# Performance work log

Hardware: AMD Instinct MI355X
Metric: run time of the kernel (lower is better)

Reference implementation:

```python
import jax, jax.numpy as jnp
import numpy as np

C_Q = 256
C_KV = 256
C_HID = 32
N_HEADS = 8
INF = 1e9


def setup_inputs() -> dict:
    key = jax.random.key(0)
    ks = jax.random.split(key, 9)
    B, Q, KV = 4, 2048, 2048
    d = N_HEADS * C_HID
    glorot_q = (6.0 / (C_Q + d)) ** 0.5
    glorot_kv = (6.0 / (C_KV + d)) ** 0.5
    return {
        "input_q": jax.random.normal(ks[0], (B, Q, C_Q), dtype=jnp.float32),
        "input_kv": jax.random.normal(ks[1], (B, KV, C_KV), dtype=jnp.float32),
        "mask": jax.random.randint(ks[2], (B, 1, 1, KV), 0, 2).astype(jnp.float32),
        "bias": jax.random.normal(ks[3], (1, N_HEADS, Q, KV), dtype=jnp.float32),
        "w_q": jax.random.uniform(ks[4], (C_Q, d), jnp.float32, -glorot_q, glorot_q),
        "w_k": jax.random.uniform(ks[5], (C_KV, d), jnp.float32, -glorot_kv, glorot_kv),
        "w_v": jax.random.uniform(ks[6], (C_KV, d), jnp.float32, -glorot_kv, glorot_kv),
        "w_o": jnp.zeros((d, C_Q), dtype=jnp.float32),  # 'final' init -> zeros
        "b_o": jnp.zeros((C_Q,), dtype=jnp.float32),
    }


def reference(input_q, input_kv, mask, bias, w_q, w_k, w_v, w_o, b_o):
    B, Q, _ = input_q.shape
    KV = input_kv.shape[1]
    # project and split heads: [B, H, L, c]
    q = (input_q @ w_q).reshape(B, Q, N_HEADS, C_HID).transpose(0, 2, 1, 3)
    k = (input_kv @ w_k).reshape(B, KV, N_HEADS, C_HID).transpose(0, 2, 1, 3)
    v = (input_kv @ w_v).reshape(B, KV, N_HEADS, C_HID).transpose(0, 2, 1, 3)
    q = q / jnp.sqrt(jnp.asarray(C_HID, q.dtype))
    # scores [B, H, Q, KV] with mask-bias and additive bias before softmax
    a = jnp.einsum("bhqc,bhkc->bhqk", q, k)
    a = a + (mask - 1.0) * INF
    if bias is not None:
        a = a + bias
    a = jax.nn.softmax(a, axis=-1)
    out = jnp.einsum("bhqk,bhkc->bhqc", a, v)  # [B, H, Q, c]
    out = out.transpose(0, 2, 1, 3).reshape(B, Q, N_HEADS * C_HID)
    return out @ w_o + b_o
```

## Files before the change

### kernel.cpp

```cpp
#include <hip/hip_runtime.h>
#include <hip/hip_bf16.h>
#include <math.h>

#define B    4
#define QL   2048
#define KVL  2048
#define CQ   256
#define CKV  256
#define CH   32
#define NH   8
#define DM   256
#define QB   128
#define KVB  128
#define NSPLIT 2
#define NS2  (KVL / KVB / NSPLIT)
#define BH   (B * NH)

typedef __attribute__((ext_vector_type(8)))  short short8;
typedef __attribute__((ext_vector_type(4)))  float f32x4;
typedef __attribute__((ext_vector_type(16))) float f32x16;
typedef __attribute__((ext_vector_type(4)))  unsigned int u32x4;

static __device__ __forceinline__ short f2bf(float x) {
    __hip_bfloat16 h = __float2bfloat16(x);
    return __builtin_bit_cast(short, h);
}
static __device__ __forceinline__ unsigned int pkbf(float lo, float hi) {
    return (unsigned int)(unsigned short)f2bf(lo) |
           ((unsigned int)(unsigned short)f2bf(hi) << 16);
}

__global__ __launch_bounds__(256) void prep_cvt(
    const float* __restrict__ src, short* __restrict__ dst, int n8)
{
    int i = blockIdx.x * 256 + threadIdx.x;
    if (i >= n8) return;
    const float4* s = (const float4*)src + (size_t)i * 2;
    float4 a = s[0], b = s[1];
    short8 o = { f2bf(a.x), f2bf(a.y), f2bf(a.z), f2bf(a.w),
                 f2bf(b.x), f2bf(b.y), f2bf(b.z), f2bf(b.w) };
    *((short8*)dst + i) = o;
}

__global__ __launch_bounds__(256) void prep_wT(
    const float* __restrict__ w, short* __restrict__ wt, int K, int N)
{
    __shared__ float tile[32][33];
    const int bx = blockIdx.x * 32;
    const int by = blockIdx.y * 32;
    const int tx = threadIdx.x & 31, ty = threadIdx.x >> 5;
    #pragma unroll
    for (int i = 0; i < 32; i += 8)
        tile[ty + i][tx] = w[(size_t)(by + ty + i) * N + bx + tx];
    __syncthreads();
    #pragma unroll
    for (int i = 0; i < 32; i += 8)
        wt[(size_t)(bx + ty + i) * K + by + tx] = f2bf(tile[tx][ty + i]);
}

__global__ __launch_bounds__(256) void gemm_mfma(
    const short* __restrict__ A, const short* __restrict__ BT,
    const float* __restrict__ bias, float* __restrict__ outf,
    short* __restrict__ outb,
    int M, int N, int K, float alpha, int mode)
{
    __shared__ __align__(16) short As[64][40];
    __shared__ __align__(16) short Bs[64][40];

    const int t   = threadIdx.x;
    const int m0  = blockIdx.y * 64, n0 = blockIdx.x * 64;
    const int lane = t & 63, w = t >> 6;
    const int c16 = lane & 15, g = lane >> 4;
    const int wm  = (w & 1) * 32, wn = (w >> 1) * 32;
    const int lr  = t >> 2, lc = (t & 3) * 8;

    f32x4 acc[2][2] = {};

    for (int k0 = 0; k0 < K; k0 += 32) {
        __syncthreads();
        *(short8*)&As[lr][lc] = *(const short8*)(A  + (size_t)(m0 + lr) * K + k0 + lc);
        *(short8*)&Bs[lr][lc] = *(const short8*)(BT + (size_t)(n0 + lr) * K + k0 + lc);
        __syncthreads();

        short8 af[2], bf[2];
        #pragma unroll
        for (int i = 0; i < 2; i++) {
            af[i] = *(const short8*)&As[wm + i * 16 + c16][g * 8];
            bf[i] = *(const short8*)&Bs[wn + i * 16 + c16][g * 8];
        }
        #pragma unroll
        for (int i = 0; i < 2; i++)
            #pragma unroll
            for (int j = 0; j < 2; j++)
                acc[i][j] = __builtin_amdgcn_mfma_f32_16x16x32_bf16(af[i], bf[j], acc[i][j], 0, 0, 0);
    }

    #pragma unroll
    for (int i = 0; i < 2; i++) {
        #pragma unroll
        for (int j = 0; j < 2; j++) {
            #pragma unroll
            for (int r = 0; r < 4; r++) {
                int m = m0 + wm + i * 16 + g * 4 + r;
                int n = n0 + wn + j * 16 + c16;
                float v = acc[i][j][r] * alpha;
                if (mode == 0) {
                    outf[(size_t)m * N + n] = v + (bias ? bias[n] : 0.0f);
                } else {
                    int bb = m >> 11, l = m & 2047;
                    int hh = n >> 5,  cc = n & 31;
                    if (mode == 1)
                        outb[(((size_t)bb * NH + hh) * QL + l) * CH + cc] = f2bf(v);
                    else
                        outb[(((size_t)bb * NH + hh) * CH + cc) * (size_t)KVL + l] = f2bf(v);
                }
            }
        }
    }
}

__global__ __launch_bounds__(256) void fattn(
    const short* __restrict__ qbf, const short* __restrict__ kbf,
    const short* __restrict__ vtb, const float* __restrict__ mask,
    const float* __restrict__ bias, float* __restrict__ opart,
    float* __restrict__ lpart)
{
    __shared__ __align__(16) short Kl[2][KVB * 32];
    __shared__ __align__(16) short Vl[2][32 * KVB];
    __shared__ __align__(16) float Ml[KVL / NSPLIT];

    const int t    = threadIdx.x;
    const int wv   = t >> 6;
    const int lane = t & 63;
    const int l31  = lane & 31;
    const int hi   = lane >> 5;

    const int s  = blockIdx.x & 1;
    const int q0 = (blockIdx.x >> 1) * QB;
    const int h  = blockIdx.y, b = blockIdx.z;
    const int bh = b * NH + h;
    const int kvbase = s * (KVL / NSPLIT);

    constexpr float L2E  = 1.4426950408889634f;
    constexpr float MBIG = 1e9f * L2E;
    constexpr float MOFF = -(1e9f * L2E) - 40.0f * L2E;

    const short* qrow = qbf + ((size_t)bh * QL + q0 + wv * 32 + l31) * CH;
    short8 qf0 = *(const short8*)(qrow + hi * 8);
    short8 qf1 = *(const short8*)(qrow + 16 + hi * 8);

    {
        float4 mv = *(const float4*)(mask + (size_t)b * KVL + kvbase + t * 4);
        float4 o0 = { fmaf(mv.x, MBIG, MOFF), fmaf(mv.y, MBIG, MOFF),
                      fmaf(mv.z, MBIG, MOFF), fmaf(mv.w, MBIG, MOFF) };
        *(float4*)&Ml[t * 4] = o0;
    }

    const int rowK = t >> 1, halfK = t & 1;
    const short* ksrc = kbf + (size_t)bh * KVL * CH + (size_t)(kvbase + rowK) * CH + halfK * 16;
    const int kb0 = (rowK * 64 + halfK * 32)      ^ ((rowK & 7) << 4);
    const int kb1 = (rowK * 64 + halfK * 32 + 16) ^ ((rowK & 7) << 4);
    const int rowV = t >> 3, segV = t & 7;
    const short* vsrc = vtb + (size_t)bh * CH * KVL + (size_t)rowV * KVL + kvbase + segV * 16;
    const int vb0 = (rowV * 256 + segV * 32)      ^ ((rowV & 7) << 4);
    const int vb1 = (rowV * 256 + segV * 32 + 16) ^ ((rowV & 7) << 4);

    short8 kr0 = *(const short8*)ksrc;
    short8 kr1 = *(const short8*)(ksrc + 8);
    short8 vr0 = *(const short8*)vsrc;
    short8 vr1 = *(const short8*)(vsrc + 8);

    const float* brow = bias + ((size_t)h * QL + q0 + wv * 32 + l31) * KVL + kvbase;

    float4 biA[4], biB[4];
    #pragma unroll
    for (int rr = 0; rr < 4; ++rr)
        biA[rr] = *(const float4*)(brow + rr * 8 + hi * 4);

    f32x16 O;
    #pragma unroll
    for (int r = 0; r < 16; ++r) O[r] = 0.0f;
    float lp0 = 0.f, lp1 = 0.f, lp2 = 0.f, lp3 = 0.f;

#define SUB_BODY(SUB, BC, BN)                                                  \
    {                                                                          \
        if ((SUB) < 3 || it + 1 < NS2) {                                       \
            _Pragma("unroll")                                                  \
            for (int rr = 0; rr < 4; ++rr)                                     \
                BN[rr] = *(const float4*)(brow + kv0 + ((SUB) + 1) * 32 + rr * 8 + hi * 4); \
        }                                                                      \
        f32x16 Cb;                                                             \
        _Pragma("unroll")                                                      \
        for (int rr = 0; rr < 4; ++rr) {                                       \
            float4 mt = *(const float4*)&Ml[kv0 + (SUB) * 32 + rr * 8 + hi * 4]; \
            Cb[4 * rr + 0] = fmaf(BC[rr].x, L2E, mt.x);                        \
            Cb[4 * rr + 1] = fmaf(BC[rr].y, L2E, mt.y);                        \
            Cb[4 * rr + 2] = fmaf(BC[rr].z, L2E, mt.z);                        \
            Cb[4 * rr + 3] = fmaf(BC[rr].w, L2E, mt.w);                        \
        }                                                                      \
        const int krow32 = (SUB) * 32 + l31;                                   \
        const int kswz   = (krow32 & 7) << 4;                                  \
        short8 ka0 = *(const short8*)(klb + ((krow32 * 64 + hi * 16) ^ kswz)); \
        short8 ka1 = *(const short8*)(klb + ((krow32 * 64 + 32 + hi * 16) ^ kswz)); \
        __builtin_amdgcn_s_setprio(1);                                         \
        f32x16 S = __builtin_amdgcn_mfma_f32_32x32x16_bf16(ka0, qf0, Cb, 0, 0, 0); \
        S = __builtin_amdgcn_mfma_f32_32x32x16_bf16(ka1, qf1, S, 0, 0, 0);     \
        __builtin_amdgcn_s_setprio(0);                                         \
        float p[16];                                                           \
        _Pragma("unroll")                                                      \
        for (int r = 0; r < 16; ++r) p[r] = __builtin_amdgcn_exp2f(S[r]);      \
        lp0 += (p[0] + p[1]) + (p[4] + p[5]);                                  \
        lp1 += (p[2] + p[3]) + (p[6] + p[7]);                                  \
        lp2 += (p[8] + p[9]) + (p[12] + p[13]);                                \
        lp3 += (p[10] + p[11]) + (p[14] + p[15]);                              \
        unsigned int a1 = pkbf(p[0], p[1]),   a2 = pkbf(p[2], p[3]);           \
        unsigned int b1 = pkbf(p[4], p[5]),   b2 = pkbf(p[6], p[7]);           \
        unsigned int c1 = pkbf(p[8], p[9]),   c2 = pkbf(p[10], p[11]);         \
        unsigned int d1 = pkbf(p[12], p[13]), d2 = pkbf(p[14], p[15]);         \
        asm("v_permlane32_swap_b32 %0, %1" : "+v"(a1), "+v"(b1));              \
        asm("v_permlane32_swap_b32 %0, %1" : "+v"(a2), "+v"(b2));              \
        asm("v_permlane32_swap_b32 %0, %1" : "+v"(c1), "+v"(d1));              \
        asm("v_permlane32_swap_b32 %0, %1" : "+v"(c2), "+v"(d2));              \
        u32x4 f0 = { a1, a2, b1, b2 };                                         \
        u32x4 f1 = { c1, c2, d1, d2 };                                         \
        short8 pf0 = __builtin_bit_cast(short8, f0);                           \
        short8 pf1 = __builtin_bit_cast(short8, f1);                           \
        const int vswz = (l31 & 7) << 4;                                       \
        short8 vf0 = *(const short8*)(vlb + ((l31 * 256 + (SUB) * 64 + hi * 16) ^ vswz)); \
        short8 vf1 = *(const short8*)(vlb + ((l31 * 256 + (SUB) * 64 + 32 + hi * 16) ^ vswz)); \
        __builtin_amdgcn_s_setprio(1);                                         \
        O = __builtin_amdgcn_mfma_f32_32x32x16_bf16(pf0, vf0, O, 0, 0, 0);     \
        O = __builtin_amdgcn_mfma_f32_32x32x16_bf16(pf1, vf1, O, 0, 0, 0);     \
        __builtin_amdgcn_s_setprio(0);                                         \
    }

    #pragma unroll 1
    for (int it = 0; it < NS2; ++it) {
        const int kv0 = it * KVB;
        char* klb = (char*)Kl[it & 1];
        char* vlb = (char*)Vl[it & 1];

        *(short8*)(klb + kb0) = kr0;
        *(short8*)(klb + kb1) = kr1;
        *(short8*)(vlb + vb0) = vr0;
        *(short8*)(vlb + vb1) = vr1;
        __syncthreads();

        if (it + 1 < NS2) {
            const short* kn = ksrc + (size_t)(it + 1) * KVB * CH;
            const short* vn = vsrc + (it + 1) * KVB;
            kr0 = *(const short8*)kn;  kr1 = *(const short8*)(kn + 8);
            vr0 = *(const short8*)vn;  vr1 = *(const short8*)(vn + 8);
        }

        SUB_BODY(0, biA, biB);
        SUB_BODY(1, biB, biA);
        SUB_BODY(2, biA, biB);
        SUB_BODY(3, biB, biA);
    }
#undef SUB_BODY

    float lpq = (lp0 + lp1) + (lp2 + lp3);
    lpq += __shfl_xor(lpq, 32);
    float* op = opart + (((size_t)s * BH + bh) * QL + q0 + wv * 32) * CH;
    #pragma unroll
    for (int r = 0; r < 16; ++r) {
        int q = (r & 3) + 8 * (r >> 2) + 4 * hi;
        op[(size_t)q * CH + l31] = O[r];
    }
    if (lane < 32)
        lpart[((size_t)s * BH + bh) * QL + q0 + wv * 32 + l31] = lpq;
}

__global__ __launch_bounds__(256) void combine(
    const float* __restrict__ opart, const float* __restrict__ lpart,
    short* __restrict__ aob)
{
    const size_t BHQ = (size_t)BH * QL;
    int i  = blockIdx.x * 256 + threadIdx.x;
    int c8 = i & 3;
    int q  = (i >> 2) & (QL - 1);
    int bh = i >> 13;
    int b  = bh >> 3, h = bh & 7;

    float l0 = lpart[(size_t)bh * QL + q];
    float l1 = lpart[BHQ + (size_t)bh * QL + q];
    float inv = 1.0f / (l0 + l1);

    size_t base = ((size_t)bh * QL + q) * CH + c8 * 8;
    const float4* oa = (const float4*)(opart + base);
    const float4* ob = (const float4*)(opart + BHQ * CH + base);
    float4 x0 = oa[0], x1 = oa[1];
    float4 y0 = ob[0], y1 = ob[1];
    short8 o = { f2bf((x0.x + y0.x) * inv), f2bf((x0.y + y0.y) * inv),
                 f2bf((x0.z + y0.z) * inv), f2bf((x0.w + y0.w) * inv),
                 f2bf((x1.x + y1.x) * inv), f2bf((x1.y + y1.y) * inv),
                 f2bf((x1.z + y1.z) * inv), f2bf((x1.w + y1.w) * inv) };
    *(short8*)(aob + ((size_t)b * QL + q) * DM + h * CH + c8 * 8) = o;
}

extern "C" void kernel_launch(void* const* d_in, const int* in_sizes, int n_in,
                              void* d_out, int out_size, void* d_ws, size_t ws_size,
                              hipStream_t stream)
{
    const float* input_q  = (const float*)d_in[0];
    const float* input_kv = (const float*)d_in[1];
    const float* mask     = (const float*)d_in[2];
    const float* bias     = (const float*)d_in[3];
    const float* w_q      = (const float*)d_in[4];
    const float* w_k      = (const float*)d_in[5];
    const float* w_v      = (const float*)d_in[6];
    const float* w_o      = (const float*)d_in[7];
    const float* b_o      = (const float*)d_in[8];
    float* out = (float*)d_out;

    const size_t TOK  = (size_t)B * QL;
    const size_t HEAD = (size_t)B * NH * QL * CH;

    short* qbf = (short*)d_ws;
    short* kbf = qbf + HEAD;
    short* vtb = kbf + HEAD;
    short* aob = vtb + HEAD;
    short* qx  = aob + HEAD;
    short* kvx = qx  + HEAD;
    short* wqT = kvx + HEAD;
    short* wkT = wqT + CQ * DM;
    short* wvT = wkT + CKV * DM;
    short* woT = wvT + CKV * DM;
    float* opart = (float*)(woT + DM * CQ);
    float* lpart = opart + 2 * (size_t)BH * QL * CH;

    dim3 blk(256);
    const float qscale = 0.17677669529663687f * 1.4426950408889634f;

    prep_cvt<<<dim3((TOK * CQ / 8 + 255) / 256), blk, 0, stream>>>(input_q,  qx,  (int)(TOK * CQ / 8));
    prep_cvt<<<dim3((TOK * CKV / 8 + 255) / 256), blk, 0, stream>>>(input_kv, kvx, (int)(TOK * CKV / 8));
    prep_wT<<<dim3(DM / 32, CQ / 32),  blk, 0, stream>>>(w_q, wqT, CQ,  DM);
    prep_wT<<<dim3(DM / 32, CKV / 32), blk, 0, stream>>>(w_k, wkT, CKV, DM);
    prep_wT<<<dim3(DM / 32, CKV / 32), blk, 0, stream>>>(w_v, wvT, CKV, DM);
    prep_wT<<<dim3(CQ / 32, DM / 32),  blk, 0, stream>>>(w_o, woT, DM,  CQ);

    dim3 pgrid(DM / 64, TOK / 64);
    gemm_mfma<<<pgrid, blk, 0, stream>>>(qx,  wqT, nullptr, nullptr, qbf,
                                         (int)TOK, DM, CQ,  qscale, 1);
    gemm_mfma<<<pgrid, blk, 0, stream>>>(kvx, wkT, nullptr, nullptr, kbf,
                                         (int)TOK, DM, CKV, 1.0f, 1);
    gemm_mfma<<<pgrid, blk, 0, stream>>>(kvx, wvT, nullptr, nullptr, vtb,
                                         (int)TOK, DM, CKV, 1.0f, 2);

    fattn<<<dim3(NSPLIT * QL / QB, NH, B), blk, 0, stream>>>(
        qbf, kbf, vtb, mask, bias, opart, lpart);

    combine<<<dim3((unsigned)((size_t)BH * QL * 4 / 256)), blk, 0, stream>>>(
        opart, lpart, aob);

    gemm_mfma<<<dim3(CQ / 64, TOK / 64), blk, 0, stream>>>(aob, woT, b_o, out, nullptr,
                                         (int)TOK, CQ, DM, 1.0f, 0);
}
```

Measured before the change: 138.2 us.

## Fuse split-KV combine into attention via intra-block wave split

Replaces the two-way split-KV attention grid plus separate combine kernel with 512-thread blocks in which two wave groups each handle half of every 128-wide KV strip, then reduce their partial outputs and row sums through shared memory and write normalized bf16 directly. This removes the fp32 partial output round trip to global memory and one kernel launch. Each block now walks the full KV length, so blocks are longer and fewer in number, and two extra block syncs are added at the end.

```diff
diff --git a/kernel.cpp b/kernel.cpp
--- a/kernel.cpp
+++ b/kernel.cpp
@@ -12,9 +12,7 @@
 #define DM   256
 #define QB   128
 #define KVB  128
-#define NSPLIT 2
-#define NS2  (KVL / KVB / NSPLIT)
-#define BH   (B * NH)
+#define NSTRIP (KVL / KVB)
 
 typedef __attribute__((ext_vector_type(8)))  short short8;
 typedef __attribute__((ext_vector_type(4)))  float f32x4;
@@ -119,86 +117,82 @@
     }
 }
 
-__global__ __launch_bounds__(256) void fattn(
+__global__ __launch_bounds__(512) void fattn(
     const short* __restrict__ qbf, const short* __restrict__ kbf,
     const short* __restrict__ vtb, const float* __restrict__ mask,
-    const float* __restrict__ bias, float* __restrict__ opart,
-    float* __restrict__ lpart)
+    const float* __restrict__ bias, short* __restrict__ aob)
 {
     __shared__ __align__(16) short Kl[2][KVB * 32];
     __shared__ __align__(16) short Vl[2][32 * KVB];
-    __shared__ __align__(16) float Ml[KVL / NSPLIT];
+    __shared__ __align__(16) float Ml[KVL];
 
     const int t    = threadIdx.x;
-    const int wv   = t >> 6;
+    const int w    = t >> 6;
+    const int wq   = w & 3;
+    const int ws   = w >> 2;
     const int lane = t & 63;
     const int l31  = lane & 31;
     const int hi   = lane >> 5;
 
-    const int s  = blockIdx.x & 1;
-    const int q0 = (blockIdx.x >> 1) * QB;
+    const int q0 = blockIdx.x * QB;
     const int h  = blockIdx.y, b = blockIdx.z;
     const int bh = b * NH + h;
-    const int kvbase = s * (KVL / NSPLIT);
+    const int ws64 = ws * 64;
 
     constexpr float L2E  = 1.4426950408889634f;
     constexpr float MBIG = 1e9f * L2E;
     constexpr float MOFF = -(1e9f * L2E) - 40.0f * L2E;
 
-    const short* qrow = qbf + ((size_t)bh * QL + q0 + wv * 32 + l31) * CH;
+    const short* qrow = qbf + ((size_t)bh * QL + q0 + wq * 32 + l31) * CH;
     short8 qf0 = *(const short8*)(qrow + hi * 8);
     short8 qf1 = *(const short8*)(qrow + 16 + hi * 8);
 
     {
-        float4 mv = *(const float4*)(mask + (size_t)b * KVL + kvbase + t * 4);
+        float4 mv = *(const float4*)(mask + (size_t)b * KVL + t * 4);
         float4 o0 = { fmaf(mv.x, MBIG, MOFF), fmaf(mv.y, MBIG, MOFF),
                       fmaf(mv.z, MBIG, MOFF), fmaf(mv.w, MBIG, MOFF) };
         *(float4*)&Ml[t * 4] = o0;
     }
 
-    const int rowK = t >> 1, halfK = t & 1;
-    const short* ksrc = kbf + (size_t)bh * KVL * CH + (size_t)(kvbase + rowK) * CH + halfK * 16;
-    const int kb0 = (rowK * 64 + halfK * 32)      ^ ((rowK & 7) << 4);
-    const int kb1 = (rowK * 64 + halfK * 32 + 16) ^ ((rowK & 7) << 4);
-    const int rowV = t >> 3, segV = t & 7;
-    const short* vsrc = vtb + (size_t)bh * CH * KVL + (size_t)rowV * KVL + kvbase + segV * 16;
-    const int vb0 = (rowV * 256 + segV * 32)      ^ ((rowV & 7) << 4);
-    const int vb1 = (rowV * 256 + segV * 32 + 16) ^ ((rowV & 7) << 4);
+    const int rowK = t >> 2, kch = t & 3;
+    const short* ksrc = kbf + (size_t)bh * KVL * CH + (size_t)rowK * CH + kch * 8;
+    const int kbyte = (rowK * 64 + kch * 16) ^ ((rowK & 7) << 4);
+    const int rowV = t >> 4, segV = t & 15;
+    const short* vsrc = vtb + (size_t)bh * CH * KVL + (size_t)rowV * KVL + segV * 8;
+    const int vbyte = (rowV * 256 + segV * 16) ^ ((rowV & 7) << 4);
 
     short8 kr0 = *(const short8*)ksrc;
-    short8 kr1 = *(const short8*)(ksrc + 8);
     short8 vr0 = *(const short8*)vsrc;
-    short8 vr1 = *(const short8*)(vsrc + 8);
-
-    const float* brow = bias + ((size_t)h * QL + q0 + wv * 32 + l31) * KVL + kvbase;
+
+    const float* brow = bias + ((size_t)h * QL + q0 + wq * 32 + l31) * KVL;
 
     float4 biA[4], biB[4];
     #pragma unroll
     for (int rr = 0; rr < 4; ++rr)
-        biA[rr] = *(const float4*)(brow + rr * 8 + hi * 4);
+        biA[rr] = *(const float4*)(brow + ws64 + rr * 8 + hi * 4);
 
     f32x16 O;
     #pragma unroll
     for (int r = 0; r < 16; ++r) O[r] = 0.0f;
     float lp0 = 0.f, lp1 = 0.f, lp2 = 0.f, lp3 = 0.f;
 
-#define SUB_BODY(SUB, BC, BN)                                                  \
+#define SUB_BODY(SO32, BC, BN, NEXTCOL, GUARD)                                 \
     {                                                                          \
-        if ((SUB) < 3 || it + 1 < NS2) {                                       \
+        if (GUARD) {                                                           \
             _Pragma("unroll")                                                  \
             for (int rr = 0; rr < 4; ++rr)                                     \
-                BN[rr] = *(const float4*)(brow + kv0 + ((SUB) + 1) * 32 + rr * 8 + hi * 4); \
+                BN[rr] = *(const float4*)(brow + (NEXTCOL) + rr * 8 + hi * 4); \
         }                                                                      \
         f32x16 Cb;                                                             \
         _Pragma("unroll")                                                      \
         for (int rr = 0; rr < 4; ++rr) {                                       \
-            float4 mt = *(const float4*)&Ml[kv0 + (SUB) * 32 + rr * 8 + hi * 4]; \
+            float4 mt = *(const float4*)&Ml[kv0 + (SO32) + rr * 8 + hi * 4];   \
             Cb[4 * rr + 0] = fmaf(BC[rr].x, L2E, mt.x);                        \
             Cb[4 * rr + 1] = fmaf(BC[rr].y, L2E, mt.y);                        \
             Cb[4 * rr + 2] = fmaf(BC[rr].z, L2E, mt.z);                        \
             Cb[4 * rr + 3] = fmaf(BC[rr].w, L2E, mt.w);                        \
         }                                                                      \
-        const int krow32 = (SUB) * 32 + l31;                                   \
+        const int krow32 = (SO32) + l31;                                       \
         const int kswz   = (krow32 & 7) << 4;                                  \
         short8 ka0 = *(const short8*)(klb + ((krow32 * 64 + hi * 16) ^ kswz)); \
         short8 ka1 = *(const short8*)(klb + ((krow32 * 64 + 32 + hi * 16) ^ kswz)); \
@@ -221,13 +215,13 @@
         asm("v_permlane32_swap_b32 %0, %1" : "+v"(a2), "+v"(b2));              \
         asm("v_permlane32_swap_b32 %0, %1" : "+v"(c1), "+v"(d1));              \
         asm("v_permlane32_swap_b32 %0, %1" : "+v"(c2), "+v"(d2));              \
-        u32x4 f0 = { a1, a2, b1, b2 };                                         \
-        u32x4 f1 = { c1, c2, d1, d2 };                                         \
-        short8 pf0 = __builtin_bit_cast(short8, f0);                           \
-        short8 pf1 = __builtin_bit_cast(short8, f1);                           \
+        u32x4 f0v = { a1, a2, b1, b2 };                                        \
+        u32x4 f1v = { c1, c2, d1, d2 };                                        \
+        short8 pf0 = __builtin_bit_cast(short8, f0v);                          \
+        short8 pf1 = __builtin_bit_cast(short8, f1v);                          \
         const int vswz = (l31 & 7) << 4;                                       \
-        short8 vf0 = *(const short8*)(vlb + ((l31 * 256 + (SUB) * 64 + hi * 16) ^ vswz)); \
-        short8 vf1 = *(const short8*)(vlb + ((l31 * 256 + (SUB) * 64 + 32 + hi * 16) ^ vswz)); \
+        short8 vf0 = *(const short8*)(vlb + ((l31 * 256 + (SO32) * 2 + hi * 16) ^ vswz)); \
+        short8 vf1 = *(const short8*)(vlb + ((l31 * 256 + (SO32) * 2 + 32 + hi * 16) ^ vswz)); \
         __builtin_amdgcn_s_setprio(1);                                         \
         O = __builtin_amdgcn_mfma_f32_32x32x16_bf16(pf0, vf0, O, 0, 0, 0);     \
         O = __builtin_amdgcn_mfma_f32_32x32x16_bf16(pf1, vf1, O, 0, 0, 0);     \
@@ -235,68 +229,54 @@
     }
 
     #pragma unroll 1
-    for (int it = 0; it < NS2; ++it) {
+    for (int it = 0; it < NSTRIP; ++it) {
         const int kv0 = it * KVB;
         char* klb = (char*)Kl[it & 1];
         char* vlb = (char*)Vl[it & 1];
 
-        *(short8*)(klb + kb0) = kr0;
-        *(short8*)(klb + kb1) = kr1;
-        *(short8*)(vlb + vb0) = vr0;
-        *(short8*)(vlb + vb1) = vr1;
+        *(short8*)(klb + kbyte) = kr0;
+        *(short8*)(vlb + vbyte) = vr0;
         __syncthreads();
 
-        if (it + 1 < NS2) {
-            const short* kn = ksrc + (size_t)(it + 1) * KVB * CH;
-            const short* vn = vsrc + (it + 1) * KVB;
-            kr0 = *(const short8*)kn;  kr1 = *(const short8*)(kn + 8);
-            vr0 = *(const short8*)vn;  vr1 = *(const short8*)(vn + 8);
-        }
-
-        SUB_BODY(0, biA, biB);
-        SUB_BODY(1, biB, biA);
-        SUB_BODY(2, biA, biB);
-        SUB_BODY(3, biB, biA);
+        if (it + 1 < NSTRIP) {
+            kr0 = *(const short8*)(ksrc + (size_t)(it + 1) * KVB * CH);
+            vr0 = *(const short8*)(vsrc + (it + 1) * KVB);
+        }
+
+        SUB_BODY(ws64,      biA, biB, kv0 + ws64 + 32,  1);
+        SUB_BODY(ws64 + 32, biB, biA, kv0 + KVB + ws64, (it + 1 < NSTRIP));
     }
 #undef SUB_BODY
 
     float lpq = (lp0 + lp1) + (lp2 + lp3);
     lpq += __shfl_xor(lpq, 32);
-    float* op = opart + (((size_t)s * BH + bh) * QL + q0 + wv * 32) * CH;
-    #pragma unroll
-    for (int r = 0; r < 16; ++r) {
-        int q = (r & 3) + 8 * (r >> 2) + 4 * hi;
-        op[(size_t)q * CH + l31] = O[r];
-    }
-    if (lane < 32)
-        lpart[((size_t)s * BH + bh) * QL + q0 + wv * 32 + l31] = lpq;
-}
-
-__global__ __launch_bounds__(256) void combine(
-    const float* __restrict__ opart, const float* __restrict__ lpart,
-    short* __restrict__ aob)
-{
-    const size_t BHQ = (size_t)BH * QL;
-    int i  = blockIdx.x * 256 + threadIdx.x;
-    int c8 = i & 3;
-    int q  = (i >> 2) & (QL - 1);
-    int bh = i >> 13;
-    int b  = bh >> 3, h = bh & 7;
-
-    float l0 = lpart[(size_t)bh * QL + q];
-    float l1 = lpart[BHQ + (size_t)bh * QL + q];
-    float inv = 1.0f / (l0 + l1);
-
-    size_t base = ((size_t)bh * QL + q) * CH + c8 * 8;
-    const float4* oa = (const float4*)(opart + base);
-    const float4* ob = (const float4*)(opart + BHQ * CH + base);
-    float4 x0 = oa[0], x1 = oa[1];
-    float4 y0 = ob[0], y1 = ob[1];
-    short8 o = { f2bf((x0.x + y0.x) * inv), f2bf((x0.y + y0.y) * inv),
-                 f2bf((x0.z + y0.z) * inv), f2bf((x0.w + y0.w) * inv),
-                 f2bf((x1.x + y1.x) * inv), f2bf((x1.y + y1.y) * inv),
-                 f2bf((x1.z + y1.z) * inv), f2bf((x1.w + y1.w) * inv) };
-    *(short8*)(aob + ((size_t)b * QL + q) * DM + h * CH + c8 * 8) = o;
+
+    float* Ob = (float*)&Kl[0][0];
+    float* Lb = (float*)&Vl[0][0];
+    __syncthreads();
+    if (ws == 1) {
+        float* op = Ob + wq * 32 * 32;
+        #pragma unroll
+        for (int r = 0; r < 16; ++r) {
+            int q = (r & 3) + 8 * (r >> 2) + 4 * hi;
+            op[q * 32 + l31] = O[r];
+        }
+        if (lane < 32) Lb[wq * 32 + l31] = lpq;
+    }
+    __syncthreads();
+    if (ws == 0) {
+        const float* op = Ob + wq * 32 * 32;
+        float ltot = lpq + Lb[wq * 32 + l31];
+        float linv = 1.0f / ltot;
+        short* aop = aob + ((size_t)b * QL + q0 + wq * 32) * DM + h * CH;
+        #pragma unroll
+        for (int r = 0; r < 16; ++r) {
+            int q = (r & 3) + 8 * (r >> 2) + 4 * hi;
+            float ov = O[r] + op[q * 32 + l31];
+            float inv = __shfl(linv, q);
+            aop[(size_t)q * DM + l31] = f2bf(ov * inv);
+        }
+    }
 }
 
 extern "C" void kernel_launch(void* const* d_in, const int* in_sizes, int n_in,
@@ -327,8 +307,6 @@
     short* wkT = wqT + CQ * DM;
     short* wvT = wkT + CKV * DM;
     short* woT = wvT + CKV * DM;
-    float* opart = (float*)(woT + DM * CQ);
-    float* lpart = opart + 2 * (size_t)BH * QL * CH;
 
     dim3 blk(256);
     const float qscale = 0.17677669529663687f * 1.4426950408889634f;
@@ -348,11 +326,8 @@
     gemm_mfma<<<pgrid, blk, 0, stream>>>(kvx, wvT, nullptr, nullptr, vtb,
                                          (int)TOK, DM, CKV, 1.0f, 2);
 
-    fattn<<<dim3(NSPLIT * QL / QB, NH, B), blk, 0, stream>>>(
-        qbf, kbf, vtb, mask, bias, opart, lpart);
-
-    combine<<<dim3((unsigned)((size_t)BH * QL * 4 / 256)), blk, 0, stream>>>(
-        opart, lpart, aob);
+    fattn<<<dim3(QL / QB, NH, B), dim3(512), 0, stream>>>(
+        qbf, kbf, vtb, mask, bias, aob);
 
     gemm_mfma<<<dim3(CQ / 64, TOK / 64), blk, 0, stream>>>(aob, woT, b_o, out, nullptr,
                                          (int)TOK, CQ, DM, 1.0f, 0);
```

Result: faster. 125.0 us (-9.5%).
